# Optimization experiments

Hardware: AMD Instinct MI355X
Metric: run time of the kernel (lower is better)

## Reference

```python
import jax, jax.numpy as jnp
import numpy as np

D_MODEL = 1024
N_HEADS = 16
D_HEAD = D_MODEL // N_HEADS
WIN = 128        # local_window
HALF = WIN // 2  # 64
KW = 2 * WIN     # kv window length per block (half-left + block + half-right)


def setup_inputs() -> dict:
    key = jax.random.key(0)
    ks = jax.random.split(key, 6)
    B, L = 2, 8192
    s = 0.02
    return {
        "x": jax.random.normal(ks[0], (B, L, D_MODEL), dtype=jnp.float32),
        "wq": jax.random.normal(ks[1], (D_MODEL, D_MODEL), dtype=jnp.float32) * s,
        "wk": jax.random.normal(ks[2], (D_MODEL, D_MODEL), dtype=jnp.float32) * s,
        "wv": jax.random.normal(ks[3], (D_MODEL, D_MODEL), dtype=jnp.float32) * s,
        "wo": jax.random.normal(ks[4], (D_MODEL, D_MODEL), dtype=jnp.float32) * s,
        "bo": jax.random.normal(ks[5], (D_MODEL,), dtype=jnp.float32) * s,
    }


def _rotate_half(t):
    t1, t2 = jnp.split(t, 2, axis=-1)
    return jnp.concatenate([-t2, t1], axis=-1)


def _rope(L, dtype):
    inv_freq = 1.0 / (10000.0 ** (jnp.arange(0, D_HEAD, 2, dtype=jnp.float32) / D_HEAD))
    t = jnp.arange(L, dtype=jnp.float32)
    freqs = t[:, None] * inv_freq[None, :]          # [L, D_HEAD/2]
    emb = jnp.concatenate([freqs, freqs], axis=-1)  # [L, D_HEAD]
    return jnp.cos(emb).astype(dtype), jnp.sin(emb).astype(dtype)


def reference(x, wq, wk, wv, wo, bo):
    B, L, D = x.shape
    H, Dh = N_HEADS, D_HEAD
    # projections (torch Linear: x @ W.T)
    q = (x @ wq.T).reshape(B, L, H, Dh).transpose(0, 2, 1, 3)  # [B,H,L,Dh]
    k = (x @ wk.T).reshape(B, L, H, Dh).transpose(0, 2, 1, 3)
    v = (x @ wv.T).reshape(B, L, H, Dh).transpose(0, 2, 1, 3)
    cos, sin = _rope(L, x.dtype)                    # [L, Dh]
    q = q * cos + _rotate_half(q) * sin
    k = k * cos + _rotate_half(k) * sin
    nb = L // WIN
    starts = jnp.arange(nb) * WIN - HALF            # window start per block
    idx = starts[:, None] + jnp.arange(KW)          # [nb, KW] kv indices
    valid = (idx >= 0) & (idx < L)
    idxc = jnp.clip(idx, 0, L - 1)
    kw = k[:, :, idxc]                              # [B,H,nb,KW,Dh]
    vw = v[:, :, idxc]
    qb = q.reshape(B, H, nb, WIN, Dh)
    scores = jnp.einsum('bhnqd,bhnkd->bhnqk', qb, kw) / np.sqrt(Dh).astype(x.dtype)
    scores = jnp.where(valid[None, None, :, None, :], scores, -jnp.inf)
    attn = jax.nn.softmax(scores, axis=-1)
    out = jnp.einsum('bhnqk,bhnkd->bhnqd', attn, vw).reshape(B, H, L, Dh)
    out = out.transpose(0, 2, 1, 3).reshape(B, L, D)
    return out @ wo.T + bo
```

## Files before the change

kernel.cpp:

```cpp
#include <hip/hip_runtime.h>
#include <cstdint>
#include <math.h>

#define L_SEQ 8192
#define DM    1024
#define NQK   2048

typedef unsigned short u16;
typedef __bf16 bf16;
typedef bf16  bf16x8 __attribute__((ext_vector_type(8)));
typedef float f32x4  __attribute__((ext_vector_type(4)));

__device__ __forceinline__ u16 f2bf(float f) {
    unsigned u = __float_as_uint(f);
    u += 0x7fffu + ((u >> 16) & 1u);
    return (u16)(u >> 16);
}

__device__ __forceinline__ f32x4 mfma16(bf16x8 a, bf16x8 b, f32x4 c) {
    return __builtin_amdgcn_mfma_f32_16x16x32_bf16(a, b, c, 0, 0, 0);
}

__device__ __forceinline__ void gld_lds16(const u16* g, u16* l) {
    __builtin_amdgcn_global_load_lds((const __attribute__((address_space(1))) void*)g,
                                     (__attribute__((address_space(3))) void*)l,
                                     16, 0, 0);
}

__device__ __forceinline__ void bar() {
    __builtin_amdgcn_s_barrier();
}
#define VMCNT4() asm volatile("s_waitcnt vmcnt(4)" ::: "memory")
#define VMCNT0() asm volatile("s_waitcnt vmcnt(0)" ::: "memory")

__global__ void cvt_bf16(const float* __restrict__ src, u16* __restrict__ dst, int n8) {
    int i = blockIdx.x * 256 + threadIdx.x;
    if (i >= n8) return;
    const float4* s4 = (const float4*)src;
    float4 a = s4[2 * i], b = s4[2 * i + 1];
    union { uint4 u; u16 h[8]; } r;
    r.h[0] = f2bf(a.x); r.h[1] = f2bf(a.y); r.h[2] = f2bf(a.z); r.h[3] = f2bf(a.w);
    r.h[4] = f2bf(b.x); r.h[5] = f2bf(b.y); r.h[6] = f2bf(b.z); r.h[7] = f2bf(b.w);
    ((uint4*)dst)[i] = r.u;
}

__global__ void rope_tbl(float2* __restrict__ t) {
    int idx = blockIdx.x * 256 + threadIdx.x;
    int pos = idx >> 5, i = idx & 31;
    float invf = exp2f(-0.4152410118609191f * (float)i);
    float s, c;
    sincosf((float)pos * invf, &s, &c);
    t[idx] = make_float2(c, s);
}


#define STAGE_A(kt, ha, par) do { \
    gld_lds16(baseA + (size_t)(ha) * 131072 + (size_t)(kt) * 64, \
              ldsA + (par) * 16384 + (ha) * 8192); \
    gld_lds16(baseA + (size_t)(ha) * 131072 + 65536 + (size_t)(kt) * 64, \
              ldsA + (par) * 16384 + (ha) * 8192 + 4096); \
} while (0)
#define STAGE_B(kt, hb, par) do { \
    gld_lds16(baseB + (size_t)(hb) * 131072 + (size_t)(kt) * 64, \
              ldsB + (par) * 16384 + (hb) * 8192); \
    gld_lds16(baseB + (size_t)(hb) * 131072 + 65536 + (size_t)(kt) * 64, \
              ldsB + (par) * 16384 + (hb) * 8192 + 4096); \
} while (0)

__global__ __launch_bounds__(512, 2) void gemm_qkv_fused(
    const u16* __restrict__ X,
    const u16* __restrict__ W,
    const float2* __restrict__ rope,
    u16* __restrict__ Y,
    u16* __restrict__ Vt)
{
    __shared__ __align__(16) u16 smem[65536];
    u16* SA = smem;
    u16* SB = smem + 32768;

    {
    }
    const int o   = (int)blockIdx.x;
    const int xcd = o & 7;
    const int r   = o >> 3;
    const int st  = r >> 5;
    const int t   = r & 31;
    const int m0  = (xcd * 8 + (t & 7)) * 256;
    const int n0  = (st * 4 + (t >> 3)) * 256;

    const int tid = threadIdx.x;
    const int lane = tid & 63, w = tid >> 6;
    const int wm = w >> 2, wn = w & 3;
    const int quad = lane >> 4, ln = lane & 15;

    const int r0 = tid >> 3;
    const int cgs = (tid & 7) ^ (r0 & 7);
    const u16* baseA = X + (size_t)(m0 + r0) * DM + cgs * 8;
    const u16* baseB = W + (size_t)(n0 + r0) * DM + cgs * 8;
    u16* ldsA = SA + tid * 8;
    u16* ldsB = SB + tid * 8;

    const int c0 = (quad ^ (ln & 7)) * 8;
    const int c1 = ((quad + 4) ^ (ln & 7)) * 8;
    const int aoff = wm * 8192 + ln * 64;
    const int boff = (wn >> 1) * 8192 + ((wn & 1) * 64 + ln) * 64;

    const f32x4 fz = {0.f, 0.f, 0.f, 0.f};
    f32x4 acc[8][4];
    #pragma unroll
    for (int a = 0; a < 8; a++)
        #pragma unroll
        for (int b = 0; b < 4; b++) acc[a][b] = fz;

    STAGE_A(0, 0, 0); STAGE_A(0, 1, 0);
    STAGE_B(0, 0, 0); STAGE_B(0, 1, 0);
    STAGE_B(1, 0, 1); STAGE_B(1, 1, 1);
    VMCNT4();
    bar();

    #pragma unroll 2
    for (int u = 0; u < 16; ++u) {
        const int par = u & 1;
        const u16* pa = SA + par * 16384 + aoff;
        const u16* pb = SB + par * 16384 + boff;
        bf16x8 af[4][2], bf[4][2];

        #pragma unroll
        for (int m = 0; m < 4; m++) {
            af[m][0] = *(const bf16x8*)(pa + m * 1024 + c0);
            af[m][1] = *(const bf16x8*)(pa + m * 1024 + c1);
        }
        #pragma unroll
        for (int n = 0; n < 2; n++) {
            bf[n][0] = *(const bf16x8*)(pb + n * 1024 + c0);
            bf[n][1] = *(const bf16x8*)(pb + n * 1024 + c1);
        }
        STAGE_A((u + 1) & 15, 0, par ^ 1);
        bar();
        __builtin_amdgcn_s_setprio(1);
        #pragma unroll
        for (int m = 0; m < 4; m++)
            #pragma unroll
            for (int n = 0; n < 2; n++) {
                acc[m][n] = mfma16(af[m][0], bf[n][0], acc[m][n]);
                acc[m][n] = mfma16(af[m][1], bf[n][1], acc[m][n]);
            }
        __builtin_amdgcn_s_setprio(0);
        bar();

        #pragma unroll
        for (int n = 0; n < 2; n++) {
            bf[2 + n][0] = *(const bf16x8*)(pb + (2 + n) * 1024 + c0);
            bf[2 + n][1] = *(const bf16x8*)(pb + (2 + n) * 1024 + c1);
        }
        STAGE_A((u + 1) & 15, 1, par ^ 1);
        bar();
        __builtin_amdgcn_s_setprio(1);
        #pragma unroll
        for (int m = 0; m < 4; m++)
            #pragma unroll
            for (int n = 0; n < 2; n++) {
                acc[m][2 + n] = mfma16(af[m][0], bf[2 + n][0], acc[m][2 + n]);
                acc[m][2 + n] = mfma16(af[m][1], bf[2 + n][1], acc[m][2 + n]);
            }
        __builtin_amdgcn_s_setprio(0);
        bar();

        #pragma unroll
        for (int m = 0; m < 4; m++) {
            af[m][0] = *(const bf16x8*)(pa + (4 + m) * 1024 + c0);
            af[m][1] = *(const bf16x8*)(pa + (4 + m) * 1024 + c1);
        }
        STAGE_B((u + 2) & 15, 0, par);
        bar();
        __builtin_amdgcn_s_setprio(1);
        #pragma unroll
        for (int m = 0; m < 4; m++)
            #pragma unroll
            for (int n = 0; n < 2; n++) {
                acc[4 + m][2 + n] = mfma16(af[m][0], bf[2 + n][0], acc[4 + m][2 + n]);
                acc[4 + m][2 + n] = mfma16(af[m][1], bf[2 + n][1], acc[4 + m][2 + n]);
            }
        __builtin_amdgcn_s_setprio(0);
        bar();

        STAGE_B((u + 2) & 15, 1, par);
        VMCNT4();
        bar();
        __builtin_amdgcn_s_setprio(1);
        #pragma unroll
        for (int m = 0; m < 4; m++)
            #pragma unroll
            for (int n = 0; n < 2; n++) {
                acc[4 + m][n] = mfma16(af[m][0], bf[n][0], acc[4 + m][n]);
                acc[4 + m][n] = mfma16(af[m][1], bf[n][1], acc[4 + m][n]);
            }
        __builtin_amdgcn_s_setprio(0);
        bar();
    }
    VMCNT0();
    bar();

    if (n0 < 2048) {
        #pragma unroll
        for (int mt = 0; mt < 8; mt++)
            #pragma unroll
            for (int reg = 0; reg < 4; reg++) {
                int rg = (m0 + wm * 128 + mt * 16 + quad * 4 + reg) & (L_SEQ - 1);
                const float2* rp = rope + rg * 32;
                #pragma unroll
                for (int nt = 0; nt < 2; nt++) {
                    float2 cs = rp[nt * 16 + ln];
                    float x1 = acc[mt][nt][reg], x2 = acc[mt][nt + 2][reg];
                    acc[mt][nt][reg]     = x1 * cs.x - x2 * cs.y;
                    acc[mt][nt + 2][reg] = x2 * cs.x + x1 * cs.y;
                }
            }
        u16* Es = smem;
        #pragma unroll
        for (int mh = 0; mh < 2; mh++) {
            if (mh) __syncthreads();
            if (wm == mh) {
                #pragma unroll
                for (int mt = 0; mt < 8; mt++)
                    #pragma unroll
                    for (int nt = 0; nt < 4; nt++)
                        #pragma unroll
                        for (int reg = 0; reg < 4; reg++)
                            Es[(mt * 16 + quad * 4 + reg) * 264 + wn * 64 + nt * 16 + ln] =
                                f2bf(acc[mt][nt][reg]);
            }
            __syncthreads();
            #pragma unroll
            for (int i = 0; i < 8; i++) {
                int idx = i * 512 + tid;
                int row = idx >> 5, ch = (idx & 31) * 8;
                uint4 v = *(const uint4*)(Es + row * 264 + ch);
                *(uint4*)(Y + (size_t)(m0 + mh * 128 + row) * NQK + n0 + ch) = v;
            }
        }
    } else {
        u16* Es = smem;
        const int bb = m0 >> 13, seq0 = m0 & (L_SEQ - 1);
        #pragma unroll
        for (int nh = 0; nh < 2; nh++) {
            if (nh) __syncthreads();
            if ((wn >> 1) == nh) {
                #pragma unroll
                for (int mt = 0; mt < 8; mt++)
                    #pragma unroll
                    for (int nt = 0; nt < 4; nt++)
                        #pragma unroll
                        for (int reg = 0; reg < 4; reg++)
                            Es[((wn & 1) * 64 + nt * 16 + ln) * 264 + wm * 128 + mt * 16 + quad * 4 + reg] =
                                f2bf(acc[mt][nt][reg]);
            }
            __syncthreads();
            #pragma unroll
            for (int i = 0; i < 8; i++) {
                int idx = i * 512 + tid;
                int dr = idx >> 5, ch = (idx & 31) * 8;
                int gc = n0 - 2048 + nh * 128 + dr;
                uint4 v = *(const uint4*)(Es + dr * 264 + ch);
                *(uint4*)(Vt + (size_t)(bb * 1024 + gc) * L_SEQ + seq0 + ch) = v;
            }
        }
    }
}

__global__ __launch_bounds__(512, 2) void gemm_oproj(
    const u16* __restrict__ A,
    const u16* __restrict__ Wo,
    const float* __restrict__ bias,
    float* __restrict__ Out)
{
    __shared__ __align__(16) u16 smem[65536];
    u16* SA = smem;
    u16* SB = smem + 32768;

    const int o   = (int)blockIdx.x;
    const int xcd = o & 7;
    const int t   = o >> 3;
    const int m0  = (xcd * 8 + (t & 7)) * 256;
    const int n0  = (t >> 3) * 256;

    const int tid = threadIdx.x;
    const int lane = tid & 63, w = tid >> 6;
    const int wm = w >> 2, wn = w & 3;
    const int quad = lane >> 4, ln = lane & 15;

    const int r0 = tid >> 3;
    const int cgs = (tid & 7) ^ (r0 & 7);
    const u16* baseA = A  + (size_t)(m0 + r0) * DM + cgs * 8;
    const u16* baseB = Wo + (size_t)(n0 + r0) * DM + cgs * 8;
    u16* ldsA = SA + tid * 8;
    u16* ldsB = SB + tid * 8;

    const int c0 = (quad ^ (ln & 7)) * 8;
    const int c1 = ((quad + 4) ^ (ln & 7)) * 8;
    const int aoff = wm * 8192 + ln * 64;
    const int boff = (wn >> 1) * 8192 + ((wn & 1) * 64 + ln) * 64;

    const f32x4 fz = {0.f, 0.f, 0.f, 0.f};
    f32x4 acc[8][4];
    #pragma unroll
    for (int a = 0; a < 8; a++)
        #pragma unroll
        for (int b = 0; b < 4; b++) acc[a][b] = fz;

    STAGE_A(0, 0, 0); STAGE_A(0, 1, 0);
    STAGE_B(0, 0, 0); STAGE_B(0, 1, 0);
    STAGE_B(1, 0, 1); STAGE_B(1, 1, 1);
    VMCNT4();
    bar();

    #pragma unroll 2
    for (int u = 0; u < 16; ++u) {
        const int par = u & 1;
        const u16* pa = SA + par * 16384 + aoff;
        const u16* pb = SB + par * 16384 + boff;
        bf16x8 af[4][2], bf[4][2];

        #pragma unroll
        for (int m = 0; m < 4; m++) {
            af[m][0] = *(const bf16x8*)(pa + m * 1024 + c0);
            af[m][1] = *(const bf16x8*)(pa + m * 1024 + c1);
        }
        #pragma unroll
        for (int n = 0; n < 2; n++) {
            bf[n][0] = *(const bf16x8*)(pb + n * 1024 + c0);
            bf[n][1] = *(const bf16x8*)(pb + n * 1024 + c1);
        }
        STAGE_A((u + 1) & 15, 0, par ^ 1);
        bar();
        __builtin_amdgcn_s_setprio(1);
        #pragma unroll
        for (int m = 0; m < 4; m++)
            #pragma unroll
            for (int n = 0; n < 2; n++) {
                acc[m][n] = mfma16(af[m][0], bf[n][0], acc[m][n]);
                acc[m][n] = mfma16(af[m][1], bf[n][1], acc[m][n]);
            }
        __builtin_amdgcn_s_setprio(0);
        bar();

        #pragma unroll
        for (int n = 0; n < 2; n++) {
            bf[2 + n][0] = *(const bf16x8*)(pb + (2 + n) * 1024 + c0);
            bf[2 + n][1] = *(const bf16x8*)(pb + (2 + n) * 1024 + c1);
        }
        STAGE_A((u + 1) & 15, 1, par ^ 1);
        bar();
        __builtin_amdgcn_s_setprio(1);
        #pragma unroll
        for (int m = 0; m < 4; m++)
            #pragma unroll
            for (int n = 0; n < 2; n++) {
                acc[m][2 + n] = mfma16(af[m][0], bf[2 + n][0], acc[m][2 + n]);
                acc[m][2 + n] = mfma16(af[m][1], bf[2 + n][1], acc[m][2 + n]);
            }
        __builtin_amdgcn_s_setprio(0);
        bar();

        #pragma unroll
        for (int m = 0; m < 4; m++) {
            af[m][0] = *(const bf16x8*)(pa + (4 + m) * 1024 + c0);
            af[m][1] = *(const bf16x8*)(pa + (4 + m) * 1024 + c1);
        }
        STAGE_B((u + 2) & 15, 0, par);
        bar();
        __builtin_amdgcn_s_setprio(1);
        #pragma unroll
        for (int m = 0; m < 4; m++)
            #pragma unroll
            for (int n = 0; n < 2; n++) {
                acc[4 + m][2 + n] = mfma16(af[m][0], bf[2 + n][0], acc[4 + m][2 + n]);
                acc[4 + m][2 + n] = mfma16(af[m][1], bf[2 + n][1], acc[4 + m][2 + n]);
            }
        __builtin_amdgcn_s_setprio(0);
        bar();

        STAGE_B((u + 2) & 15, 1, par);
        VMCNT4();
        bar();
        __builtin_amdgcn_s_setprio(1);
        #pragma unroll
        for (int m = 0; m < 4; m++)
            #pragma unroll
            for (int n = 0; n < 2; n++) {
                acc[4 + m][n] = mfma16(af[m][0], bf[n][0], acc[4 + m][n]);
                acc[4 + m][n] = mfma16(af[m][1], bf[n][1], acc[4 + m][n]);
            }
        __builtin_amdgcn_s_setprio(0);
        bar();
    }
    VMCNT0();
    bar();

    float b4[4];
    #pragma unroll
    for (int nt = 0; nt < 4; nt++) b4[nt] = bias[n0 + wn * 64 + nt * 16 + ln];

    float* Ef = (float*)smem;
    #pragma unroll
    for (int mq = 0; mq < 4; mq++) {
        if (mq) __syncthreads();
        if (wm == (mq >> 1)) {
            #pragma unroll
            for (int mt = 0; mt < 4; mt++)
                #pragma unroll
                for (int nt = 0; nt < 4; nt++)
                    #pragma unroll
                    for (int reg = 0; reg < 4; reg++)
                        Ef[(mt * 16 + quad * 4 + reg) * 260 + wn * 64 + nt * 16 + ln] =
                            acc[(mq & 1) * 4 + mt][nt][reg] + b4[nt];
        }
        __syncthreads();
        #pragma unroll
        for (int i = 0; i < 8; i++) {
            int idx = i * 512 + tid;
            int row = idx >> 6, ch = (idx & 63) * 4;
            float4 v = *(const float4*)(Ef + row * 260 + ch);
            *(float4*)(Out + (size_t)(m0 + mq * 64 + row) * DM + n0 + ch) = v;
        }
    }
}

__global__ __launch_bounds__(512, 4) void attn(
    const u16* __restrict__ QK,
    const u16* __restrict__ Vt,
    u16* __restrict__ AO)
{
    __shared__ __align__(16) u16 Ks[256 * 64];
    __shared__ __align__(16) u16 Vs[64 * 256];
    __shared__ __align__(16) u16 pbuf[8][512];

    const int blk = blockIdx.x;
    const int h   = blockIdx.y;
    const int b   = blockIdx.z;
    const int tid = threadIdx.x;
    const int lane = tid & 63, w = tid >> 6;
    const int quad = lane >> 4, ln = lane & 15;
    const int wstart = blk * 128 - 64;
    const size_t bbase = (size_t)b * L_SEQ;

    const u16* Kg = QK + 1024 + h * 64;
    const u16* Vg = Vt + (size_t)(b * 1024 + h * 64) * L_SEQ;

    #pragma unroll
    for (int i = 0; i < 4; i++) {
        int c = i * 512 + tid;
        int row = c >> 3, cl = c & 7, cg = cl ^ (row & 7);
        int kr = wstart + row;
        kr = kr < 0 ? 0 : (kr > L_SEQ - 1 ? L_SEQ - 1 : kr);
        gld_lds16(Kg + (size_t)(bbase + kr) * NQK + cg * 8, Ks + c * 8);
    }
    #pragma unroll
    for (int i = 0; i < 4; i++) {
        int c = i * 512 + tid;
        int d = c >> 5, kc = c & 31, cg = kc ^ (d & 7);
        int key = wstart + cg * 8;
        key = key < 0 ? 0 : (key > L_SEQ - 8 ? L_SEQ - 8 : key);
        gld_lds16(Vg + (size_t)d * L_SEQ + key, Vs + c * 8);
    }

    const int qrow = blk * 128 + w * 16 + ln;
    const u16* qp = QK + (bbase + qrow) * NQK + h * 64 + quad * 8;
    bf16x8 aq0 = *(const bf16x8*)qp;
    bf16x8 aq1 = *(const bf16x8*)(qp + 32);
    __syncthreads();

    const f32x4 fz = {0.f, 0.f, 0.f, 0.f};
    f32x4 s[16];
    #pragma unroll
    for (int nt = 0; nt < 16; nt++) {
        int row = nt * 16 + ln;
        bf16x8 b0 = *(const bf16x8*)(Ks + row * 64 + ((quad       ^ (ln & 7)) * 8));
        bf16x8 b1 = *(const bf16x8*)(Ks + row * 64 + (((4 + quad) ^ (ln & 7)) * 8));
        f32x4 t = mfma16(aq0, b0, fz);
        t = mfma16(aq1, b1, t);
        s[nt] = t;
    }
    __syncthreads();

    const float SC = 0.125f * 1.4426950408889634f;
    float mr[4] = {-INFINITY, -INFINITY, -INFINITY, -INFINITY};
    #pragma unroll
    for (int nt = 0; nt < 16; nt++) {
        int key = wstart + nt * 16 + ln;
        bool valid = (key >= 0) && (key < L_SEQ);
        #pragma unroll
        for (int r = 0; r < 4; r++) {
            float v = valid ? s[nt][r] * SC : -INFINITY;
            s[nt][r] = v;
            mr[r] = fmaxf(mr[r], v);
        }
    }
    #pragma unroll
    for (int off = 1; off < 16; off <<= 1)
        #pragma unroll
        for (int r = 0; r < 4; r++) mr[r] = fmaxf(mr[r], __shfl_xor(mr[r], off));

    float lr[4] = {0.f, 0.f, 0.f, 0.f};
    #pragma unroll
    for (int nt = 0; nt < 16; nt++)
        #pragma unroll
        for (int r = 0; r < 4; r++) {
            float p = exp2f(s[nt][r] - mr[r]);
            s[nt][r] = p;
            lr[r] += p;
        }
    #pragma unroll
    for (int off = 1; off < 16; off <<= 1)
        #pragma unroll
        for (int r = 0; r < 4; r++) lr[r] += __shfl_xor(lr[r], off);
    float rl[4];
    #pragma unroll
    for (int r = 0; r < 4; r++) rl[r] = 1.f / lr[r];

    u16* pb = pbuf[w];
    f32x4 o[4] = {fz, fz, fz, fz};
    #pragma unroll
    for (int ks = 0; ks < 8; ks++) {
        #pragma unroll
        for (int n2 = 0; n2 < 2; n2++) {
            int nt = ks * 2 + n2;
            #pragma unroll
            for (int r = 0; r < 4; r++)
                pb[(quad * 4 + r) * 32 + ((n2 * 16 + ln) ^ (quad * 8))] = f2bf(s[nt][r]);
        }
        bf16x8 ap = *(const bf16x8*)(pb + ln * 32 + ((quad * 8) ^ (((ln >> 2) & 3) * 8)));
        #pragma unroll
        for (int dt = 0; dt < 4; dt++) {
            int d = dt * 16 + ln;
            bf16x8 vb = *(const bf16x8*)(Vs + d * 256 + (((ks * 4 + quad) ^ (ln & 7)) * 8));
            o[dt] = mfma16(ap, vb, o[dt]);
        }
    }

    u16* AOs = Ks;
    #pragma unroll
    for (int dt = 0; dt < 4; dt++)
        #pragma unroll
        for (int r = 0; r < 4; r++)
            AOs[(w * 16 + quad * 4 + r) * 72 + dt * 16 + ln] = f2bf(o[dt][r] * rl[r]);
    __syncthreads();
    #pragma unroll
    for (int i = 0; i < 2; i++) {
        int c = i * 512 + tid;
        int row = c >> 3, ch = (c & 7) * 8;
        uint4 v = *(const uint4*)(AOs + row * 72 + ch);
        *(uint4*)(AO + (bbase + blk * 128 + row) * DM + h * 64 + ch) = v;
    }
}

extern "C" void kernel_launch(void* const* d_in, const int* in_sizes, int n_in,
                              void* d_out, int out_size, void* d_ws, size_t ws_size,
                              hipStream_t stream) {
    const float* x  = (const float*)d_in[0];
    const float* wq = (const float*)d_in[1];
    const float* wk = (const float*)d_in[2];
    const float* wv = (const float*)d_in[3];
    const float* wo = (const float*)d_in[4];
    const float* bo = (const float*)d_in[5];
    float* out = (float*)d_out;

    char* ws = (char*)d_ws;
    const size_t MB = 1024 * 1024;
    u16*   xb  = (u16*)ws;
    u16*   fqk = (u16*)(ws + 32 * MB);
    u16*   vt  = (u16*)(ws + 96 * MB);
    u16*   wf  = (u16*)(ws + 128 * MB);
    float2* rt = (float2*)(ws + 134 * MB);
    u16*   wob = (u16*)(ws + 136 * MB);
    u16*   aob = xb;

    cvt_bf16<<<8192, 256, 0, stream>>>(x, xb, 2097152);
    cvt_bf16<<<512, 256, 0, stream>>>(wq, wf, 131072);
    cvt_bf16<<<512, 256, 0, stream>>>(wk, wf + 1024 * 1024, 131072);
    cvt_bf16<<<512, 256, 0, stream>>>(wv, wf + 2 * 1024 * 1024, 131072);
    cvt_bf16<<<512, 256, 0, stream>>>(wo, wob, 131072);
    rope_tbl<<<1024, 256, 0, stream>>>(rt);

    gemm_qkv_fused<<<768, 512, 0, stream>>>(xb, wf, rt, fqk, vt);
    attn<<<dim3(64, 16, 2), 512, 0, stream>>>(fqk, vt, aob);
    gemm_oproj<<<256, 512, 0, stream>>>(aob, wob, bo, out);
}
```

Measured before the change: 343.4 us.

## Restructure GEMM k-loop into two-phase register double-buffered pipeline

Replaces the four-quarter k-step in both the QKV and output GEMMs with a loop of two half-steps. Each half-step issues one full 8x4 MFMA block while the other half's LDS fragments are loaded into a second register set. Both LDS tiles are now prefetched two k-steps ahead, and there is one barrier per iteration instead of four. The aim is to cut barrier and LDS-latency stalls between MFMA bursts. The cost is a full vmcnt(0) wait every iteration and far more live fragment registers alongside the 128-float accumulator, which risks spills or lower occupancy under the 512x2 launch bounds.

After: 356.7 us. 3.9% more time.

```diff
diff --git a/kernel.cpp b/kernel.cpp
--- a/kernel.cpp
+++ b/kernel.cpp
@@ -30,8 +30,9 @@
 __device__ __forceinline__ void bar() {
     __builtin_amdgcn_s_barrier();
 }
-#define VMCNT4() asm volatile("s_waitcnt vmcnt(4)" ::: "memory")
-#define VMCNT0() asm volatile("s_waitcnt vmcnt(0)" ::: "memory")
+#define LGKMCNT0() asm volatile("s_waitcnt lgkmcnt(0)" ::: "memory")
+#define VMCNT8()  asm volatile("s_waitcnt vmcnt(8)" ::: "memory")
+#define VMCNT0()  asm volatile("s_waitcnt vmcnt(0)" ::: "memory")
 
 __global__ void cvt_bf16(const float* __restrict__ src, u16* __restrict__ dst, int n8) {
     int i = blockIdx.x * 256 + threadIdx.x;
@@ -67,6 +68,65 @@
               ldsB + (par) * 16384 + (hb) * 8192 + 4096); \
 } while (0)
 
+#define K_LOOP_PIPELINED()                                                     \
+                       \
+    STAGE_A(0, 0, 0); STAGE_A(0, 1, 0);                                        \
+    STAGE_B(0, 0, 0); STAGE_B(0, 1, 0);                                        \
+    STAGE_A(1, 0, 1); STAGE_A(1, 1, 1);                                        \
+    STAGE_B(1, 0, 1); STAGE_B(1, 1, 1);                                        \
+    VMCNT8();                                                                  \
+    bar();                                                                     \
+    bf16x8 pA[8], pB[4], qA[8], qB[4];                                         \
+    {                                                                          \
+        const u16* pa0 = SA + aoff;                                            \
+        const u16* pb0 = SB + boff;                                            \
+        _Pragma("unroll")                                                      \
+        for (int m = 0; m < 8; m++) pA[m] = *(const bf16x8*)(pa0 + m * 1024 + c0); \
+        _Pragma("unroll")                                                      \
+        for (int n = 0; n < 4; n++) pB[n] = *(const bf16x8*)(pb0 + n * 1024 + c0); \
+    }                                                                          \
+    _Pragma("unroll 2")                                                        \
+    for (int u = 0; u < 16; ++u) {                                             \
+        const int par = u & 1;                                                 \
+        const u16* pa = SA + par * 16384 + aoff;                               \
+        const u16* pb = SB + par * 16384 + boff;                               \
+        const u16* qa = SA + (par ^ 1) * 16384 + aoff;                         \
+        const u16* qb = SB + (par ^ 1) * 16384 + boff;                         \
+                                \
+        _Pragma("unroll")                                                      \
+        for (int m = 0; m < 8; m++) qA[m] = *(const bf16x8*)(pa + m * 1024 + c1); \
+        _Pragma("unroll")                                                      \
+        for (int n = 0; n < 4; n++) qB[n] = *(const bf16x8*)(pb + n * 1024 + c1); \
+        __builtin_amdgcn_s_setprio(1);                                         \
+        _Pragma("unroll")                                                      \
+        for (int m = 0; m < 8; m++)                                            \
+            _Pragma("unroll")                                                  \
+            for (int n = 0; n < 4; n++)                                        \
+                acc[m][n] = mfma16(pA[m], pB[n], acc[m][n]);                   \
+        __builtin_amdgcn_s_setprio(0);                                         \
+        LGKMCNT0();         \
+        VMCNT0();            \
+        bar();                                                                 \
+        __builtin_amdgcn_sched_barrier(0);                                     \
+         \
+        _Pragma("unroll")                                                      \
+        for (int m = 0; m < 8; m++) pA[m] = *(const bf16x8*)(qa + m * 1024 + c0); \
+        _Pragma("unroll")                                                      \
+        for (int n = 0; n < 4; n++) pB[n] = *(const bf16x8*)(qb + n * 1024 + c0); \
+        STAGE_A((u + 2) & 15, 0, par); STAGE_A((u + 2) & 15, 1, par);          \
+        STAGE_B((u + 2) & 15, 0, par); STAGE_B((u + 2) & 15, 1, par);          \
+        __builtin_amdgcn_s_setprio(1);                                         \
+        _Pragma("unroll")                                                      \
+        for (int m = 0; m < 8; m++)                                            \
+            _Pragma("unroll")                                                  \
+            for (int n = 0; n < 4; n++)                                        \
+                acc[m][n] = mfma16(qA[m], qB[n], acc[m][n]);                   \
+        __builtin_amdgcn_s_setprio(0);                                         \
+    }                                                                          \
+    VMCNT0();                                                                  \
+    LGKMCNT0();                                                                \
+    bar();
+
 __global__ __launch_bounds__(512, 2) void gemm_qkv_fused(
     const u16* __restrict__ X,
     const u16* __restrict__ W,
@@ -78,8 +138,6 @@
     u16* SA = smem;
     u16* SB = smem + 32768;
 
-    {
-    }
     const int o   = (int)blockIdx.x;
     const int xcd = o & 7;
     const int r   = o >> 3;
@@ -112,94 +170,7 @@
         #pragma unroll
         for (int b = 0; b < 4; b++) acc[a][b] = fz;
 
-    STAGE_A(0, 0, 0); STAGE_A(0, 1, 0);
-    STAGE_B(0, 0, 0); STAGE_B(0, 1, 0);
-    STAGE_B(1, 0, 1); STAGE_B(1, 1, 1);
-    VMCNT4();
-    bar();
-
-    #pragma unroll 2
-    for (int u = 0; u < 16; ++u) {
-        const int par = u & 1;
-        const u16* pa = SA + par * 16384 + aoff;
-        const u16* pb = SB + par * 16384 + boff;
-        bf16x8 af[4][2], bf[4][2];
-
-        #pragma unroll
-        for (int m = 0; m < 4; m++) {
-            af[m][0] = *(const bf16x8*)(pa + m * 1024 + c0);
-            af[m][1] = *(const bf16x8*)(pa + m * 1024 + c1);
-        }
-        #pragma unroll
-        for (int n = 0; n < 2; n++) {
-            bf[n][0] = *(const bf16x8*)(pb + n * 1024 + c0);
-            bf[n][1] = *(const bf16x8*)(pb + n * 1024 + c1);
-        }
-        STAGE_A((u + 1) & 15, 0, par ^ 1);
-        bar();
-        __builtin_amdgcn_s_setprio(1);
-        #pragma unroll
-        for (int m = 0; m < 4; m++)
-            #pragma unroll
-            for (int n = 0; n < 2; n++) {
-                acc[m][n] = mfma16(af[m][0], bf[n][0], acc[m][n]);
-                acc[m][n] = mfma16(af[m][1], bf[n][1], acc[m][n]);
-            }
-        __builtin_amdgcn_s_setprio(0);
-        bar();
-
-        #pragma unroll
-        for (int n = 0; n < 2; n++) {
-            bf[2 + n][0] = *(const bf16x8*)(pb + (2 + n) * 1024 + c0);
-            bf[2 + n][1] = *(const bf16x8*)(pb + (2 + n) * 1024 + c1);
-        }
-        STAGE_A((u + 1) & 15, 1, par ^ 1);
-        bar();
-        __builtin_amdgcn_s_setprio(1);
-        #pragma unroll
-        for (int m = 0; m < 4; m++)
-            #pragma unroll
-            for (int n = 0; n < 2; n++) {
-                acc[m][2 + n] = mfma16(af[m][0], bf[2 + n][0], acc[m][2 + n]);
-                acc[m][2 + n] = mfma16(af[m][1], bf[2 + n][1], acc[m][2 + n]);
-            }
-        __builtin_amdgcn_s_setprio(0);
-        bar();
-
-        #pragma unroll
-        for (int m = 0; m < 4; m++) {
-            af[m][0] = *(const bf16x8*)(pa + (4 + m) * 1024 + c0);
-            af[m][1] = *(const bf16x8*)(pa + (4 + m) * 1024 + c1);
-        }
-        STAGE_B((u + 2) & 15, 0, par);
-        bar();
-        __builtin_amdgcn_s_setprio(1);
-        #pragma unroll
-        for (int m = 0; m < 4; m++)
-            #pragma unroll
-            for (int n = 0; n < 2; n++) {
-                acc[4 + m][2 + n] = mfma16(af[m][0], bf[2 + n][0], acc[4 + m][2 + n]);
-                acc[4 + m][2 + n] = mfma16(af[m][1], bf[2 + n][1], acc[4 + m][2 + n]);
-            }
-        __builtin_amdgcn_s_setprio(0);
-        bar();
-
-        STAGE_B((u + 2) & 15, 1, par);
-        VMCNT4();
-        bar();
-        __builtin_amdgcn_s_setprio(1);
-        #pragma unroll
-        for (int m = 0; m < 4; m++)
-            #pragma unroll
-            for (int n = 0; n < 2; n++) {
-                acc[4 + m][n] = mfma16(af[m][0], bf[n][0], acc[4 + m][n]);
-                acc[4 + m][n] = mfma16(af[m][1], bf[n][1], acc[4 + m][n]);
-            }
-        __builtin_amdgcn_s_setprio(0);
-        bar();
-    }
-    VMCNT0();
-    bar();
+    K_LOOP_PIPELINED();
 
     if (n0 < 2048) {
         #pragma unroll
@@ -308,94 +279,7 @@
         #pragma unroll
         for (int b = 0; b < 4; b++) acc[a][b] = fz;
 
-    STAGE_A(0, 0, 0); STAGE_A(0, 1, 0);
-    STAGE_B(0, 0, 0); STAGE_B(0, 1, 0);
-    STAGE_B(1, 0, 1); STAGE_B(1, 1, 1);
-    VMCNT4();
-    bar();
-
-    #pragma unroll 2
-    for (int u = 0; u < 16; ++u) {
-        const int par = u & 1;
-        const u16* pa = SA + par * 16384 + aoff;
-        const u16* pb = SB + par * 16384 + boff;
-        bf16x8 af[4][2], bf[4][2];
-
-        #pragma unroll
-        for (int m = 0; m < 4; m++) {
-            af[m][0] = *(const bf16x8*)(pa + m * 1024 + c0);
-            af[m][1] = *(const bf16x8*)(pa + m * 1024 + c1);
-        }
-        #pragma unroll
-        for (int n = 0; n < 2; n++) {
-            bf[n][0] = *(const bf16x8*)(pb + n * 1024 + c0);
-            bf[n][1] = *(const bf16x8*)(pb + n * 1024 + c1);
-        }
-        STAGE_A((u + 1) & 15, 0, par ^ 1);
-        bar();
-        __builtin_amdgcn_s_setprio(1);
-        #pragma unroll
-        for (int m = 0; m < 4; m++)
-            #pragma unroll
-            for (int n = 0; n < 2; n++) {
-                acc[m][n] = mfma16(af[m][0], bf[n][0], acc[m][n]);
-                acc[m][n] = mfma16(af[m][1], bf[n][1], acc[m][n]);
-            }
-        __builtin_amdgcn_s_setprio(0);
-        bar();
-
-        #pragma unroll
-        for (int n = 0; n < 2; n++) {
-            bf[2 + n][0] = *(const bf16x8*)(pb + (2 + n) * 1024 + c0);
-            bf[2 + n][1] = *(const bf16x8*)(pb + (2 + n) * 1024 + c1);
-        }
-        STAGE_A((u + 1) & 15, 1, par ^ 1);
-        bar();
-        __builtin_amdgcn_s_setprio(1);
-        #pragma unroll
-        for (int m = 0; m < 4; m++)
-            #pragma unroll
-            for (int n = 0; n < 2; n++) {
-                acc[m][2 + n] = mfma16(af[m][0], bf[2 + n][0], acc[m][2 + n]);
-                acc[m][2 + n] = mfma16(af[m][1], bf[2 + n][1], acc[m][2 + n]);
-            }
-        __builtin_amdgcn_s_setprio(0);
-        bar();
-
-        #pragma unroll
-        for (int m = 0; m < 4; m++) {
-            af[m][0] = *(const bf16x8*)(pa + (4 + m) * 1024 + c0);
-            af[m][1] = *(const bf16x8*)(pa + (4 + m) * 1024 + c1);
-        }
-        STAGE_B((u + 2) & 15, 0, par);
-        bar();
-        __builtin_amdgcn_s_setprio(1);
-        #pragma unroll
-        for (int m = 0; m < 4; m++)
-            #pragma unroll
-            for (int n = 0; n < 2; n++) {
-                acc[4 + m][2 + n] = mfma16(af[m][0], bf[2 + n][0], acc[4 + m][2 + n]);
-                acc[4 + m][2 + n] = mfma16(af[m][1], bf[2 + n][1], acc[4 + m][2 + n]);
-            }
-        __builtin_amdgcn_s_setprio(0);
-        bar();
-
-        STAGE_B((u + 2) & 15, 1, par);
-        VMCNT4();
-        bar();
-        __builtin_amdgcn_s_setprio(1);
-        #pragma unroll
-        for (int m = 0; m < 4; m++)
-            #pragma unroll
-            for (int n = 0; n < 2; n++) {
-                acc[4 + m][n] = mfma16(af[m][0], bf[n][0], acc[4 + m][n]);
-                acc[4 + m][n] = mfma16(af[m][1], bf[n][1], acc[4 + m][n]);
-            }
-        __builtin_amdgcn_s_setprio(0);
-        bar();
-    }
-    VMCNT0();
-    bar();
+    K_LOOP_PIPELINED();
 
     float b4[4];
     #pragma unroll
```
